# Performance work log

Measured on AMD Instinct MI355X. Metric: run time of the kernel, lower is better.

## Reference

```python
import jax, jax.numpy as jnp
import numpy as np

BETA = 1.0
EPS_MU = 1e-6
EPS_LOG = 1e-8
D_DIM = 2048
M_EVENTS = 16384
T_HORIZON = 100


def setup_inputs() -> dict:
    key = jax.random.key(0)
    k1, k2 = jax.random.split(key)
    # sorted event times in [0, T_HORIZON)
    t_events = jnp.sort(jax.random.uniform(k1, (M_EVENTS,), jnp.float32) * T_HORIZON)
    marks = jax.random.randint(k2, (M_EVENTS,), 0, D_DIM)  # int marks in {0..D-1}
    # learned params, init exactly as in torch module
    log_mu = jnp.full((D_DIM,), -3.0, jnp.float32)
    log_alpha = jnp.full((D_DIM, D_DIM), -4.0, jnp.float32)
    return {
        "t_events": t_events,
        "marks": marks,
        "T_max": T_HORIZON,
        "log_mu": log_mu,
        "log_alpha": log_alpha,
    }


def _loglik(t_events, log_mu, log_alpha, marks, T_max, beta=BETA):
    mu = jax.nn.softplus(log_mu) + EPS_MU          # [D]
    alpha = jax.nn.softplus(log_alpha)             # [D, D]
    D = mu.shape[0]
    # dt[0] = 0 so the first step leaves S (= zeros) untouched, matching the
    # torch loop which skips decay at n == 0.
    dt = jnp.concatenate([jnp.zeros((1,), t_events.dtype), jnp.diff(t_events)])  # [M]

    def step(S, xs):
        dt_n, d = xs
        S = jnp.exp(-beta * dt_n) * S              # exponential decay of state [D]
        lam_d = mu[d] + alpha[d] @ S               # intensity at event's mark
        S = S.at[d].add(1.0)                       # self-excitation bump
        return S, jnp.log(lam_d + EPS_LOG)

    _, log_lams = jax.lax.scan(step, jnp.zeros((D,), mu.dtype), (dt, marks))

    # compensator integral term
    T = jnp.asarray(T_max, t_events.dtype)
    one_minus_exp = 1.0 - jnp.exp(-beta * (T - t_events))          # [M]
    contrib = jax.ops.segment_sum(one_minus_exp, marks, num_segments=D)  # [D]
    integral = mu * T + alpha @ (contrib / beta)                   # [D]
    return log_lams.sum() - integral.sum()


def reference(t_events, marks, T_max, log_mu, log_alpha):
    return _loglik(t_events, log_mu, log_alpha, marks, T_max)
```

## Files before the change

kernel.cpp:

```cpp
#include <hip/hip_runtime.h>
#include <math.h>

#define D_DIM 2048
#define M_EV  16384
#define LCH   32
#define CCH   (M_EV / LCH)
#define SEG   32
#define NSEG  (CCH / SEG)
#define BETA  1.0f

__device__ __forceinline__ float softplus_f(float x){
  float e = __expf(-fabsf(x));
  return fmaxf(x, 0.0f) + __logf(1.0f + e);
}

__device__ __forceinline__ unsigned short f2bf(float f){
  unsigned b = __float_as_uint(f);
  return (unsigned short)((b + 0x7FFFu + ((b >> 16) & 1u)) >> 16);
}
__device__ __forceinline__ float bf2f(unsigned short u){
  return __uint_as_float(((unsigned)u) << 16);
}

__device__ __forceinline__ float decode_T(const void* p){
  unsigned bits = *(const unsigned*)p;
  float fv = __uint_as_float(bits);
  return (fv >= 1e-3f && fv <= 1e7f) ? fv : (float)(int)bits;
}

__device__ __forceinline__ float wave_red(float v){
  #pragma unroll
  for (int o = 32; o > 0; o >>= 1) v += __shfl_down(v, o);
  return v;
}

__global__ void k_small(const float* __restrict__ t, const int* __restrict__ m,
                        const void* Tp, const float* __restrict__ log_mu,
                        float* __restrict__ muw, float* __restrict__ contrib,
                        float* __restrict__ SL, float* __restrict__ dchunk,
                        float* __restrict__ cumdec, float* __restrict__ Aseg,
                        float* __restrict__ acc){
  const int b = blockIdx.x, tid = threadIdx.x;
  if (b < 8){
    int j = b*256 + tid;
    float v = softplus_f(log_mu[j]) + 1e-6f;
    muw[j] = v;
    float s = wave_red(v);
    if ((tid & 63) == 0) atomicAdd(&acc[2], s);
  } else if (b < 72){
    int i = (b-8)*256 + tid;
    int d = m[i];
    float ti = t[i];
    float T = decode_T(Tp);
    atomicAdd(&contrib[d], 1.0f - __expf(-BETA * (T - ti)));
    int c = i >> 5;
    if (c < CCH - 1){
      float tn = t[(c+1)*LCH];
      atomicAdd(&SL[(size_t)c * D_DIM + d], __expf(-BETA * (tn - ti)));
    }
  } else {
    int c = (b-72)*256 + tid;
    float tc = t[c*LCH];
    dchunk[c] = (c < CCH-1) ? __expf(-BETA * (t[(c+1)*LCH] - tc)) : 1.0f;
    int s0c = (c >> 5) << 5;
    cumdec[c] = __expf(-BETA * (tc - t[s0c*LCH]));
    if (b == 72 && tid < NSEG){
      int s = tid;
      Aseg[s] = (s < NSEG-1)
        ? __expf(-BETA * (t[(s+1)*SEG*LCH] - t[s*SEG*LCH])) : 1.0f;
    }
  }
}

__global__ void k_scan_local(float* __restrict__ SL,
                             const float* __restrict__ dchunk,
                             float* __restrict__ Carry){
  const int tid = threadIdx.x;
  const int seg = blockIdx.x >> 3, jb = blockIdx.x & 7;
  const int j = jb*256 + tid;
  const int c0 = seg * SEG;
  const size_t base = (size_t)c0 * D_DIM + j;
  float u = 0.f;
  float cur[4], nxt[4];
  #pragma unroll
  for (int q = 0; q < 4; ++q) cur[q] = SL[base + (size_t)q * D_DIM];
  for (int g = 0; g < SEG; g += 4){
    #pragma unroll
    for (int q = 0; q < 4; ++q)
      nxt[q] = (g+4 < SEG) ? SL[base + (size_t)(g+4+q) * D_DIM] : 0.f;
    #pragma unroll
    for (int q = 0; q < 4; ++q){
      int c = c0 + g + q;
      float l = cur[q];
      SL[(size_t)c * D_DIM + j] = u;
      u = fmaf(dchunk[c], u, l);
    }
    #pragma unroll
    for (int q = 0; q < 4; ++q) cur[q] = nxt[q];
  }
  Carry[(size_t)seg * D_DIM + j] = u;
}

__global__ void k_carry_alpha(const float* __restrict__ Carry,
                              const float* __restrict__ Aseg,
                              float* __restrict__ E,
                              const float* __restrict__ la,
                              const float* __restrict__ contrib,
                              unsigned short* __restrict__ sA,
                              float* __restrict__ acc){
  const int b = blockIdx.x, tid = threadIdx.x;
  if (b < 8){
    const int j = b*256 + tid;
    float cr[NSEG];
    #pragma unroll
    for (int s = 0; s < NSEG; ++s) cr[s] = Carry[(size_t)s * D_DIM + j];
    float e = 0.f;
    #pragma unroll
    for (int s = 0; s < NSEG; ++s){
      E[(size_t)s * D_DIM + j] = e;
      e = fmaf(Aseg[s], e, cr[s]);
    }
    return;
  }
  const int nthreads = 512*256;
  int atid = (b-8)*256 + tid;
  const float4* la4 = (const float4*)la;
  ushort4* sA4 = (ushort4*)sA;
  float p = 0.f;
  #pragma unroll
  for (int u = 0; u < 8; ++u){
    int i4 = atid + u * nthreads;
    float4 x = la4[i4];
    float4 sp;
    sp.x = softplus_f(x.x); sp.y = softplus_f(x.y);
    sp.z = softplus_f(x.z); sp.w = softplus_f(x.w);
    ushort4 h;
    h.x = f2bf(sp.x); h.y = f2bf(sp.y); h.z = f2bf(sp.z); h.w = f2bf(sp.w);
    sA4[i4] = h;
    int col = (i4 * 4) & (D_DIM - 1);
    p = fmaf(sp.x, contrib[col+0], p);
    p = fmaf(sp.y, contrib[col+1], p);
    p = fmaf(sp.z, contrib[col+2], p);
    p = fmaf(sp.w, contrib[col+3], p);
  }
  __shared__ float red[4];
  float w = wave_red(p);
  int lane = tid & 63, wid = tid >> 6;
  if (lane == 0) red[wid] = w;
  __syncthreads();
  if (tid == 0) atomicAdd(&acc[1], red[0]+red[1]+red[2]+red[3]);
}

__global__ __launch_bounds__(512) void k_events(
    const float* __restrict__ t, const int* __restrict__ m,
    const unsigned short* __restrict__ sA, const float* __restrict__ muw,
    const float* __restrict__ SL, const float* __restrict__ E,
    const float* __restrict__ cumdec, float* __restrict__ acc,
    const void* Tp, float* __restrict__ out){
  __shared__ int   ml[LCH];
  __shared__ float decs[LCH];
  __shared__ float red[LCH][8];
  const int tid = threadIdx.x;
  const int c = blockIdx.x;
  const int seg = c >> 5;
  const float cd = cumdec[c];

  const float4 sv = *(const float4*)(SL + (size_t)c  * D_DIM + tid*4);
  const float4 ev = *(const float4*)(E  + (size_t)seg * D_DIM + tid*4);
  float4 s;
  s.x = fmaf(ev.x, cd, sv.x); s.y = fmaf(ev.y, cd, sv.y);
  s.z = fmaf(ev.z, cd, sv.z); s.w = fmaf(ev.w, cd, sv.w);

  if (tid < LCH){
    ml[tid] = m[c*LCH + tid];
    float tk = t[c*LCH + tid];
    float tp = (tid == 0) ? tk : t[c*LCH + tid - 1];
    decs[tid] = __expf(-BETA * (tk - tp));
  }
  __syncthreads();

  const int lane = tid & 63, wid = tid >> 6;
  const int colb = tid * 4;

  ushort4 pf0 = *(const ushort4*)(sA + (size_t)ml[0] * D_DIM + colb);
  ushort4 pf1 = *(const ushort4*)(sA + (size_t)ml[1] * D_DIM + colb);
  ushort4 pf2 = *(const ushort4*)(sA + (size_t)ml[2] * D_DIM + colb);
  ushort4 pf3 = *(const ushort4*)(sA + (size_t)ml[3] * D_DIM + colb);
  ushort4 pf4 = *(const ushort4*)(sA + (size_t)ml[4] * D_DIM + colb);
  ushort4 pf5 = *(const ushort4*)(sA + (size_t)ml[5] * D_DIM + colb);
  ushort4 pf6 = *(const ushort4*)(sA + (size_t)ml[6] * D_DIM + colb);
  ushort4 pf7 = *(const ushort4*)(sA + (size_t)ml[7] * D_DIM + colb);

#define STAGE(Q) {                                                          \
    const int kk = k + (Q);                                                 \
    const int d = ml[kk];                                                   \
    const int kn = (kk + 8 < LCH) ? kk + 8 : LCH - 1;                       \
    ushort4 nx = *(const ushort4*)(sA + (size_t)ml[kn] * D_DIM + colb);     \
    const float dec = decs[kk];                                             \
    s.x *= dec; s.y *= dec; s.z *= dec; s.w *= dec;                         \
    float p = 0.f;                                                          \
    p = fmaf(bf2f(pf##Q.x), s.x, p);                                        \
    p = fmaf(bf2f(pf##Q.y), s.y, p);                                        \
    p = fmaf(bf2f(pf##Q.z), s.z, p);                                        \
    p = fmaf(bf2f(pf##Q.w), s.w, p);                                        \
    if ((d >> 2) == tid){                                                   \
      int r = d & 3;                                                        \
      s.x += (r==0) ? 1.f : 0.f; s.y += (r==1) ? 1.f : 0.f;                 \
      s.z += (r==2) ? 1.f : 0.f; s.w += (r==3) ? 1.f : 0.f;                 \
    }                                                                       \
    float w = wave_red(p);                                                  \
    if (lane == 0) red[kk][wid] = w;                                        \
    pf##Q = nx;                                                             \
  }

  for (int k = 0; k < LCH; k += 8){
    STAGE(0) STAGE(1) STAGE(2) STAGE(3)
    STAGE(4) STAGE(5) STAGE(6) STAGE(7)
  }
#undef STAGE

  __syncthreads();
  float lg = 0.f;
  if (tid < LCH){
    const float* r = red[tid];
    float lam = muw[ml[tid]] + ((r[0]+r[1])+(r[2]+r[3]))
                             + ((r[4]+r[5])+(r[6]+r[7]));
    lg = __logf(lam + 1e-8f);
  }
  if (tid < 64){
    float w = wave_red(lg);
    if (tid == 0){
      atomicAdd(&acc[0], w);
      __threadfence();
      unsigned old = atomicAdd((unsigned*)&acc[3], 1u);
      if (old == CCH - 1){
        float a0 = atomicAdd(&acc[0], 0.0f);
        float a1 = atomicAdd(&acc[1], 0.0f);
        float a2 = atomicAdd(&acc[2], 0.0f);
        float T = decode_T(Tp);
        out[0] = a0 - (T * a2 + a1 * (1.0f / BETA));
      }
    }
  }
}

extern "C" void kernel_launch(void* const* d_in, const int* in_sizes, int n_in,
                              void* d_out, int out_size, void* d_ws, size_t ws_size,
                              hipStream_t stream) {
  const float* t_events  = (const float*)d_in[0];
  const int*   marks     = (const int*)  d_in[1];
  const void*  Tp        =               d_in[2];
  const float* log_mu    = (const float*)d_in[3];
  const float* log_alpha = (const float*)d_in[4];
  float* out = (float*)d_out;

  float* ws      = (float*)d_ws;
  float* SL      = ws;
  float* contrib = SL + (size_t)CCH * D_DIM;
  float* acc     = contrib + D_DIM;
  float* Carry   = acc + 16;
  float* E       = Carry + (size_t)NSEG * D_DIM;
  float* muw     = E + (size_t)NSEG * D_DIM;
  float* dchunk  = muw + D_DIM;
  float* cumdec  = dchunk + CCH;
  float* Aseg    = cumdec + CCH;
  unsigned short* sA = (unsigned short*)(Aseg + NSEG);

  size_t zero_floats = (size_t)CCH * D_DIM + D_DIM + 16;
  hipMemsetAsync(d_ws, 0, zero_floats * sizeof(float), stream);

  k_small      <<<74, 256, 0, stream>>>(t_events, marks, Tp, log_mu, muw,
                                        contrib, SL, dchunk, cumdec, Aseg, acc);
  k_scan_local <<<NSEG*8, 256, 0, stream>>>(SL, dchunk, Carry);
  k_carry_alpha<<<520, 256, 0, stream>>>(Carry, Aseg, E, log_alpha,
                                         contrib, sA, acc);
  k_events     <<<CCH, 512, 0, stream>>>(t_events, marks, sA, muw,
                                         SL, E, cumdec, acc, Tp, out);
}
```

Baseline: 119.6 us.

## Compute per-event intensities independently per wave via chunk-start state plus intra-chunk correction

The per-chunk event loop no longer walks the 32 events serially with block-wide decay and bump updates. Each of the 8 waves now handles 4 events on its own: it dots the alpha row with the chunk-start state staged in shared memory, scales by exp(t0 - tk), and adds a closed-form correction for the earlier in-chunk events (alpha[d][m_l] * exp(t_l - tk)). This removes the serial dependency, the per-event 8-way cross-wave reduction and the software prefetch pipeline. In exchange it adds a shared-memory staging of the state and scalar gathers into alpha rows, and relies on exp(t0 - tk) being computed directly rather than as a running product of decays.

```diff
diff --git a/kernel.cpp b/kernel.cpp
--- a/kernel.cpp
+++ b/kernel.cpp
@@ -157,89 +157,73 @@
     const float* __restrict__ SL, const float* __restrict__ E,
     const float* __restrict__ cumdec, float* __restrict__ acc,
     const void* Tp, float* __restrict__ out){
+  __shared__ float S0[D_DIM];
+  __shared__ float tl[LCH];
   __shared__ int   ml[LCH];
-  __shared__ float decs[LCH];
-  __shared__ float red[LCH][8];
+  __shared__ float wred[8];
   const int tid = threadIdx.x;
   const int c = blockIdx.x;
   const int seg = c >> 5;
   const float cd = cumdec[c];
 
-  const float4 sv = *(const float4*)(SL + (size_t)c  * D_DIM + tid*4);
-  const float4 ev = *(const float4*)(E  + (size_t)seg * D_DIM + tid*4);
-  float4 s;
-  s.x = fmaf(ev.x, cd, sv.x); s.y = fmaf(ev.y, cd, sv.y);
-  s.z = fmaf(ev.z, cd, sv.z); s.w = fmaf(ev.w, cd, sv.w);
-
+  {
+    const float4 sv = *(const float4*)(SL + (size_t)c  * D_DIM + tid*4);
+    const float4 ev = *(const float4*)(E  + (size_t)seg * D_DIM + tid*4);
+    float4 s;
+    s.x = fmaf(ev.x, cd, sv.x); s.y = fmaf(ev.y, cd, sv.y);
+    s.z = fmaf(ev.z, cd, sv.z); s.w = fmaf(ev.w, cd, sv.w);
+    *(float4*)&S0[tid*4] = s;
+  }
   if (tid < LCH){
     ml[tid] = m[c*LCH + tid];
-    float tk = t[c*LCH + tid];
-    float tp = (tid == 0) ? tk : t[c*LCH + tid - 1];
-    decs[tid] = __expf(-BETA * (tk - tp));
+    tl[tid] = t[c*LCH + tid];
   }
   __syncthreads();
 
-  const int lane = tid & 63, wid = tid >> 6;
-  const int colb = tid * 4;
-
-  ushort4 pf0 = *(const ushort4*)(sA + (size_t)ml[0] * D_DIM + colb);
-  ushort4 pf1 = *(const ushort4*)(sA + (size_t)ml[1] * D_DIM + colb);
-  ushort4 pf2 = *(const ushort4*)(sA + (size_t)ml[2] * D_DIM + colb);
-  ushort4 pf3 = *(const ushort4*)(sA + (size_t)ml[3] * D_DIM + colb);
-  ushort4 pf4 = *(const ushort4*)(sA + (size_t)ml[4] * D_DIM + colb);
-  ushort4 pf5 = *(const ushort4*)(sA + (size_t)ml[5] * D_DIM + colb);
-  ushort4 pf6 = *(const ushort4*)(sA + (size_t)ml[6] * D_DIM + colb);
-  ushort4 pf7 = *(const ushort4*)(sA + (size_t)ml[7] * D_DIM + colb);
-
-#define STAGE(Q) {                                                          \
-    const int kk = k + (Q);                                                 \
-    const int d = ml[kk];                                                   \
-    const int kn = (kk + 8 < LCH) ? kk + 8 : LCH - 1;                       \
-    ushort4 nx = *(const ushort4*)(sA + (size_t)ml[kn] * D_DIM + colb);     \
-    const float dec = decs[kk];                                             \
-    s.x *= dec; s.y *= dec; s.z *= dec; s.w *= dec;                         \
-    float p = 0.f;                                                          \
-    p = fmaf(bf2f(pf##Q.x), s.x, p);                                        \
-    p = fmaf(bf2f(pf##Q.y), s.y, p);                                        \
-    p = fmaf(bf2f(pf##Q.z), s.z, p);                                        \
-    p = fmaf(bf2f(pf##Q.w), s.w, p);                                        \
-    if ((d >> 2) == tid){                                                   \
-      int r = d & 3;                                                        \
-      s.x += (r==0) ? 1.f : 0.f; s.y += (r==1) ? 1.f : 0.f;                 \
-      s.z += (r==2) ? 1.f : 0.f; s.w += (r==3) ? 1.f : 0.f;                 \
-    }                                                                       \
-    float w = wave_red(p);                                                  \
-    if (lane == 0) red[kk][wid] = w;                                        \
-    pf##Q = nx;                                                             \
-  }
-
-  for (int k = 0; k < LCH; k += 8){
-    STAGE(0) STAGE(1) STAGE(2) STAGE(3)
-    STAGE(4) STAGE(5) STAGE(6) STAGE(7)
-  }
-#undef STAGE
-
+  const int l = tid & 63, w = tid >> 6;
+  const int l4 = l * 4;
+
+  float4 s0[8];
+  #pragma unroll
+  for (int u = 0; u < 8; ++u) s0[u] = *(const float4*)&S0[u*256 + l4];
+
+  const float t0 = tl[0];
+  float lgw = 0.f;
+  #pragma unroll
+  for (int q = 0; q < 4; ++q){
+    const int k = w*4 + q;
+    const int d = ml[k];
+    const unsigned short* row = sA + (size_t)d * D_DIM;
+    float p = 0.f;
+    #pragma unroll
+    for (int u = 0; u < 8; ++u){
+      ushort4 a = *(const ushort4*)(row + u*256 + l4);
+      p = fmaf(bf2f(a.x), s0[u].x, p);
+      p = fmaf(bf2f(a.y), s0[u].y, p);
+      p = fmaf(bf2f(a.z), s0[u].z, p);
+      p = fmaf(bf2f(a.w), s0[u].w, p);
+    }
+    const float tk = tl[k];
+    float g = 0.f;
+    if (l < k) g = bf2f(row[ml[l]]) * __expf(tl[l] - tk);
+    p = fmaf(p, __expf(t0 - tk), g);
+    float v = wave_red(p);
+    if (l == 0) lgw += __logf(muw[d] + v + 1e-8f);
+  }
+  if (l == 0) wred[w] = lgw;
   __syncthreads();
-  float lg = 0.f;
-  if (tid < LCH){
-    const float* r = red[tid];
-    float lam = muw[ml[tid]] + ((r[0]+r[1])+(r[2]+r[3]))
-                             + ((r[4]+r[5])+(r[6]+r[7]));
-    lg = __logf(lam + 1e-8f);
-  }
-  if (tid < 64){
-    float w = wave_red(lg);
-    if (tid == 0){
-      atomicAdd(&acc[0], w);
-      __threadfence();
-      unsigned old = atomicAdd((unsigned*)&acc[3], 1u);
-      if (old == CCH - 1){
-        float a0 = atomicAdd(&acc[0], 0.0f);
-        float a1 = atomicAdd(&acc[1], 0.0f);
-        float a2 = atomicAdd(&acc[2], 0.0f);
-        float T = decode_T(Tp);
-        out[0] = a0 - (T * a2 + a1 * (1.0f / BETA));
-      }
+  if (tid == 0){
+    float lg = ((wred[0]+wred[1])+(wred[2]+wred[3]))
+             + ((wred[4]+wred[5])+(wred[6]+wred[7]));
+    atomicAdd(&acc[0], lg);
+    __threadfence();
+    unsigned old = atomicAdd((unsigned*)&acc[3], 1u);
+    if (old == CCH - 1){
+      float a0 = atomicAdd(&acc[0], 0.0f);
+      float a1 = atomicAdd(&acc[1], 0.0f);
+      float a2 = atomicAdd(&acc[2], 0.0f);
+      float T = decode_T(Tp);
+      out[0] = a0 - (T * a2 + a1 * (1.0f / BETA));
     }
   }
 }
```

After: 114.5 us. -4.3%, faster.
